# Kernel tuning notes

Hardware: AMD Instinct MI355X
Metric: run time of the kernel (lower is better)

Reference implementation:

```python
import jax, jax.numpy as jnp
import numpy as np

LEVEL_SHAPES = ((128, 128), (64, 64), (32, 32), (16, 16))  # (H_l, W_l) per level
B, LQ, C, H, L, P, DFF = 4, 1024, 256, 8, 4, 4, 1024
DH = C // H
LSRC = sum(h * w for h, w in LEVEL_SHAPES)
NORMALIZER = np.array([[w, h] for h, w in LEVEL_SHAPES], dtype=np.float32)  # (L,2) as (W,H)


def layer_norm(x, g, b, eps=1e-5):
    m = jnp.mean(x, -1, keepdims=True)
    v = jnp.var(x, -1, keepdims=True)
    return (x - m) * jax.lax.rsqrt(v + eps) * g + b


def mha(tgt, query_pos, w_in, b_in, w_out, b_out):
    # nn.MultiheadAttention with q=k=tgt+pos, v=tgt (eval mode, no dropout)
    qk = tgt + query_pos
    q = (qk @ w_in[:C].T + b_in[:C]).reshape(B, LQ, H, DH)
    k = (qk @ w_in[C:2 * C].T + b_in[C:2 * C]).reshape(B, LQ, H, DH)
    v = (tgt @ w_in[2 * C:].T + b_in[2 * C:]).reshape(B, LQ, H, DH)
    att = jax.nn.softmax(jnp.einsum('bqhd,bkhd->bhqk', q, k) / np.float32(np.sqrt(DH)), axis=-1)
    o = jnp.einsum('bhqk,bkhd->bqhd', att, v).reshape(B, LQ, C)
    return o @ w_out.T + b_out


def ms_deform_attn(query, ref, src, off_w, off_b, aw_w, aw_b, val_w, val_b, out_w, out_b):
    value = (src @ val_w.T + val_b).reshape(B, LSRC, H, DH)
    offsets = (query @ off_w.T + off_b).reshape(B, LQ, H, L, P, 2)
    aw = jax.nn.softmax((query @ aw_w.T + aw_b).reshape(B, LQ, H, L * P), axis=-1)
    aw = aw.reshape(B, LQ, H, L, P)
    # sampling locations in [0,1], offsets normalized per level by (W_l, H_l)
    loc = ref[:, :, None, :, None, :] + offsets / NORMALIZER[None, None, None, :, None, :]
    out = jnp.zeros((B, LQ, H, DH), query.dtype)
    start = 0
    for l, (h, w) in enumerate(LEVEL_SHAPES):
        v = value[:, start:start + h * w].reshape(B, h, w, H, DH)
        v = v.transpose(0, 3, 1, 2, 4).reshape(B, H, h * w, DH)  # [B,H,hw,DH]
        start += h * w
        # grid_sample semantics: align_corners=False, zero padding
        x = loc[:, :, :, l, :, 0] * w - 0.5  # [B,LQ,H,P]
        y = loc[:, :, :, l, :, 1] * h - 0.5
        x0 = jnp.floor(x); y0 = jnp.floor(y)
        x0i = x0.astype(jnp.int32); y0i = y0.astype(jnp.int32)
        wx1 = x - x0; wx0 = 1.0 - wx1
        wy1 = y - y0; wy0 = 1.0 - wy1

        def gather(ix, iy):
            valid = ((ix >= 0) & (ix < w) & (iy >= 0) & (iy < h)).astype(v.dtype)
            idx = jnp.clip(iy, 0, h - 1) * w + jnp.clip(ix, 0, w - 1)
            idx = idx.transpose(0, 2, 1, 3).reshape(B, H, LQ * P)
            g = jnp.take_along_axis(v, idx[..., None], axis=2).reshape(B, H, LQ, P, DH)
            return g * valid.transpose(0, 2, 1, 3)[..., None]

        def wmul(ww):
            return ww.transpose(0, 2, 1, 3)[..., None]  # [B,H,LQ,P,1]

        s = (gather(x0i, y0i) * wmul(wx0 * wy0)
             + gather(x0i + 1, y0i) * wmul(wx1 * wy0)
             + gather(x0i, y0i + 1) * wmul(wx0 * wy1)
             + gather(x0i + 1, y0i + 1) * wmul(wx1 * wy1))
        out = out + jnp.einsum('bhqpd,bqhp->bqhd', s, aw[:, :, :, l])
    return out.reshape(B, LQ, C) @ out_w.T + out_b


def setup_inputs():
    key = jax.random.key(0)
    ks = jax.random.split(key, 16)

    def n(i, shape, s=0.02):
        return jax.random.normal(ks[i], shape, jnp.float32) * s

    z = lambda *s: jnp.zeros(s, jnp.float32)
    o = lambda *s: jnp.ones(s, jnp.float32)
    return {
        'tgt': n(0, (B, LQ, C), 1.0),
        'query_pos': n(1, (B, LQ, C), 1.0),
        'reference_points': jax.random.uniform(ks[2], (B, LQ, L, 2), jnp.float32),
        'src': n(3, (B, LSRC, C), 1.0),
        'in_w': n(4, (3 * C, C)), 'in_b': z(3 * C),
        'sa_w': n(5, (C, C)), 'sa_b': z(C),
        'off_w': n(6, (H * L * P * 2, C)), 'off_b': n(7, (H * L * P * 2,), 2.0),
        'aw_w': n(8, (H * L * P, C)), 'aw_b': z(H * L * P),
        'val_w': n(9, (C, C)), 'val_b': z(C),
        'co_w': n(10, (C, C)), 'co_b': z(C),
        'ln1_g': o(C), 'ln1_b': z(C),
        'ln2_g': o(C), 'ln2_b': z(C),
        'ln3_g': o(C), 'ln3_b': z(C),
        'f1_w': n(11, (DFF, C)), 'f1_b': z(DFF),
        'f2_w': n(12, (C, DFF)), 'f2_b': z(C),
    }


def reference(tgt, query_pos, reference_points, src, in_w, in_b, sa_w, sa_b,
              off_w, off_b, aw_w, aw_b, val_w, val_b, co_w, co_b,
              ln1_g, ln1_b, ln2_g, ln2_b, ln3_g, ln3_b,
              f1_w, f1_b, f2_w, f2_b):
    # self-attention + residual + norm2
    tgt2 = mha(tgt, query_pos, in_w, in_b, sa_w, sa_b)
    tgt = layer_norm(tgt + tgt2, ln2_g, ln2_b)
    # multi-scale deformable cross-attention + residual + norm1 (DETR path)
    tgt2 = ms_deform_attn(tgt + query_pos, reference_points, src,
                          off_w, off_b, aw_w, aw_b, val_w, val_b, co_w, co_b)
    tgt = layer_norm(tgt + tgt2, ln1_g, ln1_b)
    # FFN + residual + norm3
    tgt2 = jax.nn.relu(tgt @ f1_w.T + f1_b) @ f2_w.T + f2_b
    tgt = layer_norm(tgt + tgt2, ln3_g, ln3_b)
    return tgt
```

## Files before the change

### kernel.cpp

```cpp
#include <hip/hip_runtime.h>
#include <hip/hip_bf16.h>
#include <math.h>

#define Bv   4
#define LQv  1024
#define Cv   256
#define Hv   8
#define Lv   4
#define Pv   4
#define DFFv 1024
#define DHv  32
#define LSRCv 21760

typedef __attribute__((ext_vector_type(8))) short bhalf8;
typedef __attribute__((ext_vector_type(4))) float floatx4;

__device__ inline unsigned pk_bf16x2(float x, float y) {
    unsigned xb = __float_as_uint(x), yb = __float_as_uint(y);
    unsigned xr = (xb + 0x7FFFu + ((xb >> 16) & 1u)) >> 16;
    unsigned yr = (yb + 0x7FFFu + ((yb >> 16) & 1u)) >> 16;
    return xr | (yr << 16);
}
__device__ inline unsigned short bf16_1(float x) {
    unsigned xb = __float_as_uint(x);
    return (unsigned short)((xb + 0x7FFFu + ((xb >> 16) & 1u)) >> 16);
}
__device__ inline float ubf2f(unsigned short u) {
    return __uint_as_float(((unsigned)u) << 16);
}

__global__ __launch_bounds__(256) void cvt_weights(const float* __restrict__ in_w,
                                                   const float* __restrict__ sa_w,
                                                   const float* __restrict__ val_w,
                                                   const float* __restrict__ off_w,
                                                   const float* __restrict__ aw_w,
                                                   const float* __restrict__ co_w,
                                                   const float* __restrict__ f1_w,
                                                   const float* __restrict__ f2_w,
                                                   unsigned short* __restrict__ wp) {
    const size_t idx4 = (size_t)blockIdx.x * 256 + threadIdx.x;
    if (idx4 >= 253952) return;
    const size_t f = idx4 * 4;
    const float* src; size_t off; int K; size_t obase;
    if (f < 196608)      { src = in_w;  off = f;          K = 256;  obase = 0; }
    else if (f < 262144) { src = sa_w;  off = f - 196608; K = 256;  obase = 196608; }
    else if (f < 327680) { src = val_w; off = f - 262144; K = 256;  obase = 262144; }
    else if (f < 393216) { src = off_w; off = f - 327680; K = 256;  obase = 327680; }
    else if (f < 425984) { src = aw_w;  off = f - 393216; K = 256;  obase = 393216; }
    else if (f < 491520) { src = co_w;  off = f - 425984; K = 256;  obase = 425984; }
    else if (f < 753664) { src = f1_w;  off = f - 491520; K = 256;  obase = 491520; }
    else                 { src = f2_w;  off = f - 753664; K = 1024; obase = 753664; }
    float4 v = *(const float4*)(src + off);
    const int n = (int)(off / (size_t)K), k = (int)(off % (size_t)K);
    const size_t di = obase + ((size_t)((n >> 4) * (K >> 5) + (k >> 5))) * 512
                    + (size_t)(((k >> 3) & 3) * 128 + (n & 15) * 8 + (k & 7));
    *(uint2*)(wp + di) = (uint2){pk_bf16x2(v.x, v.y), pk_bf16x2(v.z, v.w)};
}

__global__ __launch_bounds__(256, 4) void gemm_mfma(const float* __restrict__ A,
                                                    const float* __restrict__ A2,
                                                    const unsigned short* __restrict__ Wp,
                                                    const float* __restrict__ bias,
                                                    float* __restrict__ Cf,
                                                    unsigned short* __restrict__ Ch,
                                                    int M, int N, int K, int relu) {
    __shared__ __attribute__((aligned(16))) float As[64 * 68];
    const int bm = blockIdx.y * 64;
    const int bn = blockIdx.x * 64;
    const int tid = threadIdx.x;
    const int wid = tid >> 6, lane = tid & 63;
    const int wr = wid >> 1, wc = wid & 1;
    const int col16 = lane & 15;
    const int quad = lane >> 4;

    const int srow = wid * 16 + (lane >> 4);
    const int scol = (lane & 15) * 4;
    const float* asrc = A + (size_t)(bm + srow) * K + scol;
    const float* a2src = A2 ? A2 + (size_t)(bm + srow) * K + scol : nullptr;
    float* sdst = &As[srow * 68 + scol];

    const int K32 = K >> 5;
    const unsigned short* wbase = Wp + ((size_t)((bn >> 4) + wc * 2) * K32) * 512
                                + (size_t)lane * 8;

    floatx4 acc[2][2] = {};
    float4 rv[4];

    auto loadA = [&](int c) {
#pragma unroll
        for (int i = 0; i < 4; ++i)
            rv[i] = *(const float4*)(asrc + (size_t)i * 4 * K + c * 64);
        if (a2src) {
#pragma unroll
            for (int i = 0; i < 4; ++i) {
                float4 t = *(const float4*)(a2src + (size_t)i * 4 * K + c * 64);
                rv[i].x += t.x; rv[i].y += t.y; rv[i].z += t.z; rv[i].w += t.w;
            }
        }
    };
    auto writeA = [&]() {
#pragma unroll
        for (int i = 0; i < 4; ++i)
            *(float4*)(sdst + i * 4 * 68) = rv[i];
    };

    const int NC = K >> 6;
    loadA(0);
    writeA();

    for (int c = 0; c < NC; ++c) {
        __syncthreads();
        if (c + 1 < NC) loadA(c + 1);

#pragma unroll
        for (int s = 0; s < 2; ++s) {
            bhalf8 bfr[2];
#pragma unroll
            for (int nt = 0; nt < 2; ++nt)
                bfr[nt] = *(const bhalf8*)(wbase + ((size_t)(nt * K32 + c * 2 + s)) * 512);
            bhalf8 af[2];
#pragma unroll
            for (int mt = 0; mt < 2; ++mt) {
                const float* ap = &As[(wr * 32 + mt * 16 + col16) * 68 + s * 32 + quad * 8];
                float4 lo = *(const float4*)ap;
                float4 hi = *(const float4*)(ap + 4);
                union { uint4 u; bhalf8 h; } cv;
                cv.u.x = pk_bf16x2(lo.x, lo.y);
                cv.u.y = pk_bf16x2(lo.z, lo.w);
                cv.u.z = pk_bf16x2(hi.x, hi.y);
                cv.u.w = pk_bf16x2(hi.z, hi.w);
                af[mt] = cv.h;
            }
#pragma unroll
            for (int mt = 0; mt < 2; ++mt)
#pragma unroll
                for (int nt = 0; nt < 2; ++nt)
                    acc[mt][nt] = __builtin_amdgcn_mfma_f32_16x16x32_bf16(
                        af[mt], bfr[nt], acc[mt][nt], 0, 0, 0);
        }

        __syncthreads();
        if (c + 1 < NC) writeA();
    }

#pragma unroll
    for (int mt = 0; mt < 2; ++mt) {
#pragma unroll
        for (int nt = 0; nt < 2; ++nt) {
            const int col = bn + wc * 32 + nt * 16 + col16;
            const float bv = bias[col];
#pragma unroll
            for (int i = 0; i < 4; ++i) {
                const int row = bm + wr * 32 + mt * 16 + quad * 4 + i;
                float v = acc[mt][nt][i] + bv;
                if (relu) v = fmaxf(v, 0.f);
                if (Ch) Ch[(size_t)row * N + col] = bf16_1(v);
                else    Cf[(size_t)row * N + col] = v;
            }
        }
    }
}

#define ATT_SCALE 0.17677669529663687f
__global__ __launch_bounds__(256, 2) void attn_mfma(const float* __restrict__ Q,
                                                    const float* __restrict__ Kb,
                                                    const float* __restrict__ Vb,
                                                    float* __restrict__ O,
                                                    int qk_stride) {
    const int b = blockIdx.z, h = blockIdx.y, qt = blockIdx.x;
    const int tid = threadIdx.x;
    const int wid = tid >> 6, lane = tid & 63;
    const int col16 = lane & 15, quad = lane >> 4;

    __shared__ unsigned short smem_us[40960];
    unsigned short* Ks = smem_us + wid * 9600;
    unsigned short* Vt = Ks + 2560;
    unsigned short* Ps = Ks + 4864;
    float* corr_s = (float*)(Ks + 9472);
    unsigned short* Qs = smem_us + 38400;

    {
        const int row = tid >> 2, part = tid & 3;
        const float* qsrc = Q + ((size_t)(b * LQv + qt * 64 + row)) * qk_stride + h * DHv + part * 8;
        float4 qa = *(const float4*)qsrc;
        float4 qb2 = *(const float4*)(qsrc + 4);
        uint4 qp = {pk_bf16x2(qa.x * ATT_SCALE, qa.y * ATT_SCALE),
                    pk_bf16x2(qa.z * ATT_SCALE, qa.w * ATT_SCALE),
                    pk_bf16x2(qb2.x * ATT_SCALE, qb2.y * ATT_SCALE),
                    pk_bf16x2(qb2.z * ATT_SCALE, qb2.w * ATT_SCALE)};
        *(uint4*)&Qs[row * 40 + part * 8] = qp;
    }
    __syncthreads();
    bhalf8 qfr[4];
#pragma unroll
    for (int j = 0; j < 4; ++j)
        qfr[j] = *(const bhalf8*)&Qs[(j * 16 + col16) * 40 + quad * 8];

    float m_state[4] = {-1e30f, -1e30f, -1e30f, -1e30f};
    float l_state[4] = {0.f, 0.f, 0.f, 0.f};
    floatx4 acc_o[4][2] = {};
    const int dd = lane & 31, half = lane >> 5;

    const float* kbase = Kb + ((size_t)(b * LQv + wid * 256)) * qk_stride + h * DHv;
    const float* vbase = Vb + ((size_t)(b * LQv + wid * 256)) * Cv + h * DHv;

#pragma unroll 1
    for (int t = 0; t < 4; ++t) {
        {
            const float* ks = kbase + (size_t)(t * 64 + lane) * qk_stride;
            float4 f0 = *(const float4*)(ks + 0),  f1 = *(const float4*)(ks + 4);
            float4 f2 = *(const float4*)(ks + 8),  f3 = *(const float4*)(ks + 12);
            float4 f4 = *(const float4*)(ks + 16), f5 = *(const float4*)(ks + 20);
            float4 f6 = *(const float4*)(ks + 24), f7 = *(const float4*)(ks + 28);
            uint4 p0 = {pk_bf16x2(f0.x, f0.y), pk_bf16x2(f0.z, f0.w),
                        pk_bf16x2(f1.x, f1.y), pk_bf16x2(f1.z, f1.w)};
            uint4 p1 = {pk_bf16x2(f2.x, f2.y), pk_bf16x2(f2.z, f2.w),
                        pk_bf16x2(f3.x, f3.y), pk_bf16x2(f3.z, f3.w)};
            uint4 p2 = {pk_bf16x2(f4.x, f4.y), pk_bf16x2(f4.z, f4.w),
                        pk_bf16x2(f5.x, f5.y), pk_bf16x2(f5.z, f5.w)};
            uint4 p3 = {pk_bf16x2(f6.x, f6.y), pk_bf16x2(f6.z, f6.w),
                        pk_bf16x2(f7.x, f7.y), pk_bf16x2(f7.z, f7.w)};
            *(uint4*)&Ks[lane * 40 + 0]  = p0;
            *(uint4*)&Ks[lane * 40 + 8]  = p1;
            *(uint4*)&Ks[lane * 40 + 16] = p2;
            *(uint4*)&Ks[lane * 40 + 24] = p3;
        }
        {
            const float* vs = vbase + (size_t)(t * 64 + half * 32) * Cv + dd;
#pragma unroll
            for (int j4 = 0; j4 < 8; ++j4) {
                float g0 = vs[(j4 * 4 + 0) * Cv], g1 = vs[(j4 * 4 + 1) * Cv];
                float g2 = vs[(j4 * 4 + 2) * Cv], g3 = vs[(j4 * 4 + 3) * Cv];
                uint2 vp = {pk_bf16x2(g0, g1), pk_bf16x2(g2, g3)};
                *(uint2*)&Vt[dd * 72 + half * 32 + j4 * 4] = vp;
            }
        }

        floatx4 accs[4][4] = {};
        bhalf8 af[4];
#pragma unroll
        for (int kf = 0; kf < 4; ++kf)
            af[kf] = *(const bhalf8*)&Ks[(kf * 16 + col16) * 40 + quad * 8];
#pragma unroll
        for (int kf = 0; kf < 4; ++kf)
#pragma unroll
            for (int qf = 0; qf < 4; ++qf)
                accs[kf][qf] = __builtin_amdgcn_mfma_f32_16x16x32_bf16(
                    af[kf], qfr[qf], accs[kf][qf], 0, 0, 0);

#pragma unroll
        for (int qf = 0; qf < 4; ++qf) {
            float tmax = -1e30f;
#pragma unroll
            for (int kf = 0; kf < 4; ++kf) {
                tmax = fmaxf(tmax, fmaxf(fmaxf(accs[kf][qf][0], accs[kf][qf][1]),
                                         fmaxf(accs[kf][qf][2], accs[kf][qf][3])));
            }
            tmax = fmaxf(tmax, __shfl_xor(tmax, 16));
            tmax = fmaxf(tmax, __shfl_xor(tmax, 32));
            float mnew = fmaxf(m_state[qf], tmax);
            float cr = __expf(m_state[qf] - mnew);
            m_state[qf] = mnew;
            float psum = 0.f;
#pragma unroll
            for (int kf = 0; kf < 4; ++kf) {
                float p0 = __expf(accs[kf][qf][0] - mnew);
                float p1 = __expf(accs[kf][qf][1] - mnew);
                float p2 = __expf(accs[kf][qf][2] - mnew);
                float p3 = __expf(accs[kf][qf][3] - mnew);
                psum += (p0 + p1) + (p2 + p3);
                uint2 pp = {pk_bf16x2(p0, p1), pk_bf16x2(p2, p3)};
                *(uint2*)&Ps[(qf * 16 + col16) * 72 + kf * 16 + quad * 4] = pp;
            }
            psum += __shfl_xor(psum, 16);
            psum += __shfl_xor(psum, 32);
            l_state[qf] = l_state[qf] * cr + psum;
            if (quad == 0) corr_s[qf * 16 + col16] = cr;
        }

#pragma unroll
        for (int mf = 0; mf < 4; ++mf) {
            float4 cv = *(const float4*)&corr_s[mf * 16 + quad * 4];
#pragma unroll
            for (int nf = 0; nf < 2; ++nf) {
                acc_o[mf][nf][0] *= cv.x;
                acc_o[mf][nf][1] *= cv.y;
                acc_o[mf][nf][2] *= cv.z;
                acc_o[mf][nf][3] *= cv.w;
            }
        }
#pragma unroll
        for (int ks2 = 0; ks2 < 2; ++ks2) {
            bhalf8 pf[4], vf[2];
#pragma unroll
            for (int mf = 0; mf < 4; ++mf)
                pf[mf] = *(const bhalf8*)&Ps[(mf * 16 + col16) * 72 + ks2 * 32 + quad * 8];
#pragma unroll
            for (int nf = 0; nf < 2; ++nf)
                vf[nf] = *(const bhalf8*)&Vt[(nf * 16 + col16) * 72 + ks2 * 32 + quad * 8];
#pragma unroll
            for (int mf = 0; mf < 4; ++mf)
#pragma unroll
                for (int nf = 0; nf < 2; ++nf)
                    acc_o[mf][nf] = __builtin_amdgcn_mfma_f32_16x16x32_bf16(
                        pf[mf], vf[nf], acc_o[mf][nf], 0, 0, 0);
        }
    }

    __syncthreads();
    float* mbuf = (float*)smem_us;
    float* lbuf = mbuf + 256;
    float* obuf = lbuf + 256;
    if (quad == 0) {
#pragma unroll
        for (int qf = 0; qf < 4; ++qf) {
            mbuf[wid * 64 + qf * 16 + col16] = m_state[qf];
            lbuf[wid * 64 + qf * 16 + col16] = l_state[qf];
        }
    }
#pragma unroll
    for (int mf = 0; mf < 4; ++mf)
#pragma unroll
        for (int nf = 0; nf < 2; ++nf)
#pragma unroll
            for (int i = 0; i < 4; ++i)
                obuf[wid * 2048 + (mf * 16 + quad * 4 + i) * 32 + nf * 16 + col16] =
                    acc_o[mf][nf][i];
    __syncthreads();
    {
        const int q = tid >> 2, dg = (tid & 3) * 8;
        float m0 = mbuf[q], m1 = mbuf[64 + q], m2 = mbuf[128 + q], m3 = mbuf[192 + q];
        float gm = fmaxf(fmaxf(m0, m1), fmaxf(m2, m3));
        float e0 = __expf(m0 - gm), e1 = __expf(m1 - gm);
        float e2 = __expf(m2 - gm), e3 = __expf(m3 - gm);
        float lt = lbuf[q] * e0 + lbuf[64 + q] * e1 + lbuf[128 + q] * e2 + lbuf[192 + q] * e3;
        float inv = 1.f / lt;
        const float* o0 = obuf + q * 32 + dg;
        float* orow = O + ((size_t)(b * LQv + qt * 64 + q)) * Cv + h * DHv + dg;
        float ov[8];
#pragma unroll
        for (int d = 0; d < 8; ++d)
            ov[d] = (o0[d] * e0 + o0[2048 + d] * e1 + o0[4096 + d] * e2 + o0[6144 + d] * e3) * inv;
        *(float4*)(orow) = make_float4(ov[0], ov[1], ov[2], ov[3]);
        *(float4*)(orow + 4) = make_float4(ov[4], ov[5], ov[6], ov[7]);
    }
}

__global__ __launch_bounds__(256) void deform_sample(const unsigned short* __restrict__ value,
                                                     const float* __restrict__ offs,
                                                     const float* __restrict__ awl,
                                                     const float* __restrict__ ref,
                                                     float* __restrict__ out) {
    const int bq = blockIdx.x;
    const int b = bq >> 10;
    const int tid = threadIdx.x;
    const int h = tid >> 5, d = tid & 31;

    const float* aw = awl + (size_t)bq * (Hv * Lv * Pv) + h * 16;
    float w[16];
    float mx = -1e30f;
#pragma unroll
    for (int j = 0; j < 16; ++j) { w[j] = aw[j]; mx = fmaxf(mx, w[j]); }
    float ssum = 0.f;
#pragma unroll
    for (int j = 0; j < 16; ++j) { w[j] = __expf(w[j] - mx); ssum += w[j]; }
    float invs = 1.f / ssum;

    const float* op = offs + (size_t)bq * 256 + h * 32;
    const float* rp = ref + (size_t)bq * (Lv * 2);

    const int starts[4] = {0, 16384, 20480, 21504};
    const int WHl[4] = {128, 64, 32, 16};

    float acc = 0.f;
#pragma unroll 1
    for (int l = 0; l < 4; ++l) {
        const int wl = WHl[l];
        const float rx = rp[l * 2 + 0], ry = rp[l * 2 + 1];
        const unsigned short* vb0 = value + ((size_t)b * LSRCv + starts[l]) * Cv + h * DHv + d;
#pragma unroll 1
        for (int p = 0; p < 4; ++p) {
            float ox = op[l * 8 + p * 2 + 0], oy = op[l * 8 + p * 2 + 1];
            float x = rx * (float)wl + ox - 0.5f;
            float y = ry * (float)wl + oy - 0.5f;
            float fx0 = floorf(x), fy0 = floorf(y);
            int x0 = (int)fx0, y0 = (int)fy0;
            float tx = x - fx0, ty = y - fy0;
            float w00 = (1.f - tx) * (1.f - ty);
            float w10 = tx * (1.f - ty);
            float w01 = (1.f - tx) * ty;
            float w11 = tx * ty;
            float s = 0.f;
            bool xin0 = (x0 >= 0) & (x0 < wl);
            bool xin1 = (x0 + 1 >= 0) & (x0 + 1 < wl);
            bool yin0 = (y0 >= 0) & (y0 < wl);
            bool yin1 = (y0 + 1 >= 0) & (y0 + 1 < wl);
            if (yin0) {
                if (xin0) s = fmaf(w00, ubf2f(vb0[(size_t)(y0 * wl + x0) * Cv]), s);
                if (xin1) s = fmaf(w10, ubf2f(vb0[(size_t)(y0 * wl + x0 + 1) * Cv]), s);
            }
            if (yin1) {
                if (xin0) s = fmaf(w01, ubf2f(vb0[(size_t)((y0 + 1) * wl + x0) * Cv]), s);
                if (xin1) s = fmaf(w11, ubf2f(vb0[(size_t)((y0 + 1) * wl + x0 + 1) * Cv]), s);
            }
            acc = fmaf(w[l * 4 + p] * invs, s, acc);
        }
    }
    out[(size_t)bq * Cv + h * DHv + d] = acc;
}

__global__ __launch_bounds__(256) void ln_residual(const float* __restrict__ x,
                                                   const float* __restrict__ r,
                                                   const float* __restrict__ g,
                                                   const float* __restrict__ bta,
                                                   float* __restrict__ out) {
    const int row = blockIdx.x;
    const int tid = threadIdx.x;
    float v = x[(size_t)row * Cv + tid] + r[(size_t)row * Cv + tid];
    float s = v, sq = v * v;
#pragma unroll
    for (int off = 32; off > 0; off >>= 1) {
        s  += __shfl_down(s, off, 64);
        sq += __shfl_down(sq, off, 64);
    }
    __shared__ float ss[4], sqq[4];
    int wid = tid >> 6;
    if ((tid & 63) == 0) { ss[wid] = s; sqq[wid] = sq; }
    __syncthreads();
    __shared__ float meansh, rstdsh;
    if (tid == 0) {
        float S = ss[0] + ss[1] + ss[2] + ss[3];
        float Q = sqq[0] + sqq[1] + sqq[2] + sqq[3];
        float mean = S * (1.f / Cv);
        float var = Q * (1.f / Cv) - mean * mean;
        meansh = mean;
        rstdsh = rsqrtf(var + 1e-5f);
    }
    __syncthreads();
    out[(size_t)row * Cv + tid] = (v - meansh) * rstdsh * g[tid] + bta[tid];
}

extern "C" void kernel_launch(void* const* d_in, const int* in_sizes, int n_in,
                              void* d_out, int out_size, void* d_ws, size_t ws_size,
                              hipStream_t stream) {
    const float* tgt       = (const float*)d_in[0];
    const float* query_pos = (const float*)d_in[1];
    const float* ref_pts   = (const float*)d_in[2];
    const float* src       = (const float*)d_in[3];
    const float* in_w      = (const float*)d_in[4];
    const float* in_b      = (const float*)d_in[5];
    const float* sa_w      = (const float*)d_in[6];
    const float* sa_b      = (const float*)d_in[7];
    const float* off_w     = (const float*)d_in[8];
    const float* off_b     = (const float*)d_in[9];
    const float* aw_w      = (const float*)d_in[10];
    const float* aw_b      = (const float*)d_in[11];
    const float* val_w     = (const float*)d_in[12];
    const float* val_b     = (const float*)d_in[13];
    const float* co_w      = (const float*)d_in[14];
    const float* co_b      = (const float*)d_in[15];
    const float* ln1_g     = (const float*)d_in[16];
    const float* ln1_b     = (const float*)d_in[17];
    const float* ln2_g     = (const float*)d_in[18];
    const float* ln2_b     = (const float*)d_in[19];
    const float* ln3_g     = (const float*)d_in[20];
    const float* ln3_b     = (const float*)d_in[21];
    const float* f1_w      = (const float*)d_in[22];
    const float* f1_b      = (const float*)d_in[23];
    const float* f2_w      = (const float*)d_in[24];
    const float* f2_b      = (const float*)d_in[25];

    const int M0  = Bv * LQv * Cv;
    const int VSZ = Bv * LSRCv * Cv;
    float* ws = (float*)d_ws;

    float* big    = ws;
    float* qkbuf  = big;
    float* vb     = big + (size_t)2 * M0;
    float* ob     = big + (size_t)3 * M0;
    unsigned short* value16 = (unsigned short*)big;
    unsigned short* wb = (unsigned short*)(big + (size_t)20000000);
    float* tgt_a  = ws + (size_t)VSZ;
    float* offs   = tgt_a + M0;
    float* awb    = offs + M0;
    float* sampled= awb + (size_t)Bv * LQv * 128;
    float* tgt_b  = sampled + M0;
    float* hidden = tgt_b + M0;
    float* tmp    = hidden + (size_t)Bv * LQv * DFFv;

    const size_t WB_IN = 0, WB_SA = 196608, WB_VAL = 262144, WB_OFF = 327680,
                 WB_AW = 393216, WB_CO = 425984, WB_F1 = 491520, WB_F2 = 753664;

    const int Mq = Bv * LQv;
    dim3 blk256(256);

    cvt_weights<<<dim3(992), blk256, 0, stream>>>(
        in_w, sa_w, val_w, off_w, aw_w, co_w, f1_w, f2_w, wb);

    gemm_mfma<<<dim3(512 / 64, Mq / 64), blk256, 0, stream>>>(
        tgt, query_pos, wb + WB_IN, in_b, qkbuf, nullptr, Mq, 512, Cv, 0);
    gemm_mfma<<<dim3(Cv / 64, Mq / 64), blk256, 0, stream>>>(
        tgt, nullptr, wb + WB_IN + 131072, in_b + 2 * Cv, vb, nullptr, Mq, Cv, Cv, 0);

    attn_mfma<<<dim3(LQv / 64, Hv, Bv), blk256, 0, stream>>>(qkbuf, qkbuf + 256, vb, ob, 512);

    gemm_mfma<<<dim3(Cv / 64, Mq / 64), blk256, 0, stream>>>(
        ob, nullptr, wb + WB_SA, sa_b, tmp, nullptr, Mq, Cv, Cv, 0);
    ln_residual<<<dim3(Mq), blk256, 0, stream>>>(tgt, tmp, ln2_g, ln2_b, tgt_a);

    gemm_mfma<<<dim3(Cv / 64, (Bv * LSRCv) / 64), blk256, 0, stream>>>(
        src, nullptr, wb + WB_VAL, val_b, nullptr, value16, Bv * LSRCv, Cv, Cv, 0);

    gemm_mfma<<<dim3(Cv / 64, Mq / 64), blk256, 0, stream>>>(
        tgt_a, query_pos, wb + WB_OFF, off_b, offs, nullptr, Mq, Cv, Cv, 0);
    gemm_mfma<<<dim3(128 / 64, Mq / 64), blk256, 0, stream>>>(
        tgt_a, query_pos, wb + WB_AW, aw_b, awb, nullptr, Mq, 128, Cv, 0);

    deform_sample<<<dim3(Bv * LQv), blk256, 0, stream>>>(value16, offs, awb, ref_pts, sampled);

    gemm_mfma<<<dim3(Cv / 64, Mq / 64), blk256, 0, stream>>>(
        sampled, nullptr, wb + WB_CO, co_b, tmp, nullptr, Mq, Cv, Cv, 0);
    ln_residual<<<dim3(Mq), blk256, 0, stream>>>(tgt_a, tmp, ln1_g, ln1_b, tgt_b);

    gemm_mfma<<<dim3(DFFv / 64, Mq / 64), blk256, 0, stream>>>(
        tgt_b, nullptr, wb + WB_F1, f1_b, hidden, nullptr, Mq, DFFv, Cv, 1);
    gemm_mfma<<<dim3(Cv / 64, Mq / 64), blk256, 0, stream>>>(
        hidden, nullptr, wb + WB_F2, f2_b, tmp, nullptr, Mq, Cv, DFFv, 0);
    ln_residual<<<dim3(Mq), blk256, 0, stream>>>(tgt_b, tmp, ln3_g, ln3_b, (float*)d_out);
}
```

Before: 404.5 us.

## Fuse offset and attention-weight GEMMs, remap GEMM blocks per XCD, raise occupancy

The offset and attention-weight projections now run as one 384-wide GEMM. This works by packing the aw weights after the off weights and concatenating their biases into one buffer, so deform_sample reads both from a single interleaved buffer. The GEMM grid becomes 1D, with a block-index remap that keeps row panels on the same XCD to improve L2 reuse of A. The launch-bounds minimum blocks per CU goes from 4 to 8. These cut one launch and one redundant read of the query activations, with some risk of register spilling from the tighter occupancy bound.

```diff
diff --git a/kernel.cpp b/kernel.cpp
--- a/kernel.cpp
+++ b/kernel.cpp
@@ -37,27 +37,35 @@
                                                    const float* __restrict__ co_w,
                                                    const float* __restrict__ f1_w,
                                                    const float* __restrict__ f2_w,
-                                                   unsigned short* __restrict__ wp) {
+                                                   const float* __restrict__ off_b,
+                                                   const float* __restrict__ aw_b,
+                                                   unsigned short* __restrict__ wp,
+                                                   float* __restrict__ cbias) {
     const size_t idx4 = (size_t)blockIdx.x * 256 + threadIdx.x;
-    if (idx4 >= 253952) return;
+    if (idx4 >= 253952) {
+        const int t = (int)(idx4 - 253952);
+        if (t < 256) cbias[t] = off_b[t];
+        else if (t < 384) cbias[t] = aw_b[t - 256];
+        return;
+    }
     const size_t f = idx4 * 4;
-    const float* src; size_t off; int K; size_t obase;
+    const float* src; size_t off; int K; size_t obase; int nadd = 0;
     if (f < 196608)      { src = in_w;  off = f;          K = 256;  obase = 0; }
     else if (f < 262144) { src = sa_w;  off = f - 196608; K = 256;  obase = 196608; }
     else if (f < 327680) { src = val_w; off = f - 262144; K = 256;  obase = 262144; }
     else if (f < 393216) { src = off_w; off = f - 327680; K = 256;  obase = 327680; }
-    else if (f < 425984) { src = aw_w;  off = f - 393216; K = 256;  obase = 393216; }
+    else if (f < 425984) { src = aw_w;  off = f - 393216; K = 256;  obase = 327680; nadd = 256; }
     else if (f < 491520) { src = co_w;  off = f - 425984; K = 256;  obase = 425984; }
     else if (f < 753664) { src = f1_w;  off = f - 491520; K = 256;  obase = 491520; }
     else                 { src = f2_w;  off = f - 753664; K = 1024; obase = 753664; }
     float4 v = *(const float4*)(src + off);
-    const int n = (int)(off / (size_t)K), k = (int)(off % (size_t)K);
+    const int n = (int)(off / (size_t)K) + nadd, k = (int)(off % (size_t)K);
     const size_t di = obase + ((size_t)((n >> 4) * (K >> 5) + (k >> 5))) * 512
                     + (size_t)(((k >> 3) & 3) * 128 + (n & 15) * 8 + (k & 7));
     *(uint2*)(wp + di) = (uint2){pk_bf16x2(v.x, v.y), pk_bf16x2(v.z, v.w)};
 }
 
-__global__ __launch_bounds__(256, 4) void gemm_mfma(const float* __restrict__ A,
+__global__ __launch_bounds__(256, 8) void gemm_mfma(const float* __restrict__ A,
                                                     const float* __restrict__ A2,
                                                     const unsigned short* __restrict__ Wp,
                                                     const float* __restrict__ bias,
@@ -65,8 +73,12 @@
                                                     unsigned short* __restrict__ Ch,
                                                     int M, int N, int K, int relu) {
     __shared__ __attribute__((aligned(16))) float As[64 * 68];
-    const int bm = blockIdx.y * 64;
-    const int bn = blockIdx.x * 64;
+    const unsigned bid = blockIdx.x;
+    const unsigned nc = (unsigned)N >> 6;
+    const unsigned xcd = bid & 7, j = bid >> 3;
+    const unsigned cpan = j % nc, r8 = j / nc;
+    const int bm = (int)((xcd + (r8 << 3)) << 6);
+    const int bn = (int)(cpan << 6);
     const int tid = threadIdx.x;
     const int wid = tid >> 6, lane = tid & 63;
     const int wr = wid >> 1, wc = wid & 1;
@@ -347,8 +359,7 @@
 }
 
 __global__ __launch_bounds__(256) void deform_sample(const unsigned short* __restrict__ value,
-                                                     const float* __restrict__ offs,
-                                                     const float* __restrict__ awl,
+                                                     const float* __restrict__ oab,
                                                      const float* __restrict__ ref,
                                                      float* __restrict__ out) {
     const int bq = blockIdx.x;
@@ -356,7 +367,7 @@
     const int tid = threadIdx.x;
     const int h = tid >> 5, d = tid & 31;
 
-    const float* aw = awl + (size_t)bq * (Hv * Lv * Pv) + h * 16;
+    const float* aw = oab + (size_t)bq * 384 + 256 + h * 16;
     float w[16];
     float mx = -1e30f;
 #pragma unroll
@@ -366,7 +377,7 @@
     for (int j = 0; j < 16; ++j) { w[j] = __expf(w[j] - mx); ssum += w[j]; }
     float invs = 1.f / ssum;
 
-    const float* op = offs + (size_t)bq * 256 + h * 32;
+    const float* op = oab + (size_t)bq * 384 + h * 32;
     const float* rp = ref + (size_t)bq * (Lv * 2);
 
     const int starts[4] = {0, 16384, 20480, 21504};
@@ -480,51 +491,49 @@
     float* ob     = big + (size_t)3 * M0;
     unsigned short* value16 = (unsigned short*)big;
     unsigned short* wb = (unsigned short*)(big + (size_t)20000000);
+    float* cbias  = big + (size_t)20510000;
     float* tgt_a  = ws + (size_t)VSZ;
-    float* offs   = tgt_a + M0;
-    float* awb    = offs + M0;
-    float* sampled= awb + (size_t)Bv * LQv * 128;
+    float* oabuf  = tgt_a + M0;
+    float* sampled= oabuf + (size_t)Bv * LQv * 384;
     float* tgt_b  = sampled + M0;
     float* hidden = tgt_b + M0;
     float* tmp    = hidden + (size_t)Bv * LQv * DFFv;
 
-    const size_t WB_IN = 0, WB_SA = 196608, WB_VAL = 262144, WB_OFF = 327680,
-                 WB_AW = 393216, WB_CO = 425984, WB_F1 = 491520, WB_F2 = 753664;
+    const size_t WB_IN = 0, WB_SA = 196608, WB_VAL = 262144, WB_OA = 327680,
+                 WB_CO = 425984, WB_F1 = 491520, WB_F2 = 753664;
 
     const int Mq = Bv * LQv;
     dim3 blk256(256);
 
-    cvt_weights<<<dim3(992), blk256, 0, stream>>>(
-        in_w, sa_w, val_w, off_w, aw_w, co_w, f1_w, f2_w, wb);
-
-    gemm_mfma<<<dim3(512 / 64, Mq / 64), blk256, 0, stream>>>(
+    cvt_weights<<<dim3(993), blk256, 0, stream>>>(
+        in_w, sa_w, val_w, off_w, aw_w, co_w, f1_w, f2_w, off_b, aw_b, wb, cbias);
+
+    gemm_mfma<<<dim3((Mq / 64) * (512 / 64)), blk256, 0, stream>>>(
         tgt, query_pos, wb + WB_IN, in_b, qkbuf, nullptr, Mq, 512, Cv, 0);
-    gemm_mfma<<<dim3(Cv / 64, Mq / 64), blk256, 0, stream>>>(
+    gemm_mfma<<<dim3((Mq / 64) * (Cv / 64)), blk256, 0, stream>>>(
         tgt, nullptr, wb + WB_IN + 131072, in_b + 2 * Cv, vb, nullptr, Mq, Cv, Cv, 0);
 
     attn_mfma<<<dim3(LQv / 64, Hv, Bv), blk256, 0, stream>>>(qkbuf, qkbuf + 256, vb, ob, 512);
 
-    gemm_mfma<<<dim3(Cv / 64, Mq / 64), blk256, 0, stream>>>(
+    gemm_mfma<<<dim3((Mq / 64) * (Cv / 64)), blk256, 0, stream>>>(
         ob, nullptr, wb + WB_SA, sa_b, tmp, nullptr, Mq, Cv, Cv, 0);
     ln_residual<<<dim3(Mq), blk256, 0, stream>>>(tgt, tmp, ln2_g, ln2_b, tgt_a);
 
-    gemm_mfma<<<dim3(Cv / 64, (Bv * LSRCv) / 64), blk256, 0, stream>>>(
+    gemm_mfma<<<dim3(((Bv * LSRCv) / 64) * (Cv / 64)), blk256, 0, stream>>>(
         src, nullptr, wb + WB_VAL, val_b, nullptr, value16, Bv * LSRCv, Cv, Cv, 0);
 
-    gemm_mfma<<<dim3(Cv / 64, Mq / 64), blk256, 0, stream>>>(
-        tgt_a, query_pos, wb + WB_OFF, off_b, offs, nullptr, Mq, Cv, Cv, 0);
-    gemm_mfma<<<dim3(128 / 64, Mq / 64), blk256, 0, stream>>>(
-        tgt_a, query_pos, wb + WB_AW, aw_b, awb, nullptr, Mq, 128, Cv, 0);
-
-    deform_sample<<<dim3(Bv * LQv), blk256, 0, stream>>>(value16, offs, awb, ref_pts, sampled);
-
-    gemm_mfma<<<dim3(Cv / 64, Mq / 64), blk256, 0, stream>>>(
+    gemm_mfma<<<dim3((Mq / 64) * (384 / 64)), blk256, 0, stream>>>(
+        tgt_a, query_pos, wb + WB_OA, cbias, oabuf, nullptr, Mq, 384, Cv, 0);
+
+    deform_sample<<<dim3(Bv * LQv), blk256, 0, stream>>>(value16, oabuf, ref_pts, sampled);
+
+    gemm_mfma<<<dim3((Mq / 64) * (Cv / 64)), blk256, 0, stream>>>(
         sampled, nullptr, wb + WB_CO, co_b, tmp, nullptr, Mq, Cv, Cv, 0);
     ln_residual<<<dim3(Mq), blk256, 0, stream>>>(tgt_a, tmp, ln1_g, ln1_b, tgt_b);
 
-    gemm_mfma<<<dim3(DFFv / 64, Mq / 64), blk256, 0, stream>>>(
+    gemm_mfma<<<dim3((Mq / 64) * (DFFv / 64)), blk256, 0, stream>>>(
         tgt_b, nullptr, wb + WB_F1, f1_b, hidden, nullptr, Mq, DFFv, Cv, 1);
-    gemm_mfma<<<dim3(Cv / 64, Mq / 64), blk256, 0, stream>>>(
+    gemm_mfma<<<dim3((Mq / 64) * (Cv / 64)), blk256, 0, stream>>>(
         hidden, nullptr, wb + WB_F2, f2_b, tmp, nullptr, Mq, Cv, DFFv, 0);
     ln_residual<<<dim3(Mq), blk256, 0, stream>>>(tgt_b, tmp, ln3_g, ln3_b, (float*)d_out);
 }
```

Result: slower. 439.0 us (+8.5%).
